# Kernel optimization log

Measured on AMD Instinct MI355X. Metric: run time of the kernel, lower is better.

Reference implementation:

```python
import jax, jax.numpy as jnp
import numpy as np

PAD = 0
CONST_NO = 10000   # ids > CONST_NO are variables
N_PRED = 50
B, S, G = 8, 64, 8
F, R, BMAX = 200000, 200, 3
K_F, K_R = 64, 32  # max fact / rule children per state


def _is_var(x):
    return x > CONST_NO


def setup_inputs() -> dict:
    key = jax.random.key(0)
    ks = jax.random.split(key, 12)
    # facts: (pred, arg0, arg1), preds in [1, N_PRED], args are constants
    fp = jax.random.randint(ks[0], (F, 1), 1, N_PRED + 1, dtype=jnp.int32)
    fa = jax.random.randint(ks[1], (F, 2), 1, CONST_NO + 1, dtype=jnp.int32)
    facts = jnp.concatenate([fp, fa], axis=1)
    fact_scores = jax.random.uniform(ks[2], (F,), jnp.float32, 0.1, 1.0)
    # rule heads: p(V1, V2) with V1 = CONST_NO+1, V2 = CONST_NO+2
    hp = jax.random.randint(ks[3], (R, 1), 1, N_PRED + 1, dtype=jnp.int32)
    heads = jnp.concatenate([hp,
                             jnp.full((R, 1), CONST_NO + 1, jnp.int32),
                             jnp.full((R, 1), CONST_NO + 2, jnp.int32)], axis=1)
    # rule bodies: args are head vars or fresh constants
    bp = jax.random.randint(ks[4], (R, BMAX, 1), 1, N_PRED + 1, dtype=jnp.int32)
    choice = jax.random.randint(ks[5], (R, BMAX, 2), 0, 3, dtype=jnp.int32)
    consts = jax.random.randint(ks[6], (R, BMAX, 2), 1, CONST_NO + 1, dtype=jnp.int32)
    bargs = jnp.where(choice == 0, CONST_NO + 1,
                      jnp.where(choice == 1, CONST_NO + 2, consts)).astype(jnp.int32)
    bodies = jnp.concatenate([bp, bargs], axis=2)
    rule_lens = jax.random.randint(ks[7], (R,), 1, BMAX + 1, dtype=jnp.int32)
    rule_scores = jax.random.uniform(ks[8], (R,), jnp.float32, 0.1, 1.0)
    # proof goals [B,S,G,3]: args mix of constants and query vars CONST_NO+3/+4
    gp = jax.random.randint(ks[9], (B, S, G, 1), 1, N_PRED + 1, dtype=jnp.int32)
    vch = jax.random.randint(ks[10], (B, S, G, 2), 0, 4, dtype=jnp.int32)
    gc = jax.random.randint(ks[11], (B, S, G, 2), 1, CONST_NO + 1, dtype=jnp.int32)
    gargs = jnp.where(vch == 0, CONST_NO + 3,
                      jnp.where(vch == 1, CONST_NO + 4, gc)).astype(jnp.int32)
    goals = jnp.concatenate([gp, gargs], axis=3)
    # variable number of live goals per state (tail padded)
    pos = jnp.arange(G)
    keep = jax.random.randint(jax.random.fold_in(key, 99), (B, S, 1), 1, G + 1, dtype=jnp.int32)
    goals = jnp.where(pos[None, None, :, None] < keep[..., None], goals, PAD)
    state_scores = jax.random.uniform(jax.random.fold_in(key, 7), (B, S), jnp.float32, 0.1, 1.0)
    return dict(proof_goals=goals, state_scores=state_scores, facts=facts,
                fact_scores=fact_scores, heads=heads, bodies=bodies,
                rule_lens=rule_lens, rule_scores=rule_scores)


def reference(proof_goals, state_scores, facts, fact_scores, heads, bodies, rule_lens, rule_scores):
    # ---- 1. SELECT: query = goal slot 0, remaining goals mask slot 0 ----
    q = proof_goals[:, :, 0]                         # [B,S,3]
    active = q[..., 0] != PAD                        # [B,S]
    remaining = proof_goals.at[:, :, 0, :].set(PAD)  # [B,S,G,3]
    qp, qa0, qa1 = q[..., 0], q[..., 1], q[..., 2]

    # ---- 2. RESOLVE FACTS: unify query against fact table ----
    m = ((qp[..., None] == facts[:, 0])
         & (_is_var(qa0)[..., None] | (qa0[..., None] == facts[:, 1]))
         & (_is_var(qa1)[..., None] | (qa1[..., None] == facts[:, 2]))
         & active[..., None])                        # [B,S,F]
    fvals, fidx = jax.lax.top_k(m.astype(jnp.int32), K_F)
    fact_success = fvals > 0                         # [B,S,K_f]
    mf = facts[fidx]                                 # [B,S,K_f,3]
    # substitute query variables with matched fact constants in remaining goals
    v0 = qa0[:, :, None, None, None]
    v1 = qa1[:, :, None, None, None]
    b0 = mf[..., 1][..., None, None]
    b1 = mf[..., 2][..., None, None]
    rem = remaining[:, :, None]                      # [B,S,1,G,3]
    fg = jnp.where(_is_var(v0) & (rem == v0), b0, rem)
    fg = jnp.where(_is_var(v1) & (fg == v1), b1, fg)  # [B,S,K_f,G,3]
    fsc = jnp.where(fact_success, state_scores[:, :, None] * fact_scores[fidx], 0.0)

    # ---- 3. RESOLVE RULES: unify query against rule heads, append bodies ----
    mr = ((qp[..., None] == heads[:, 0])
          & (_is_var(heads[:, 1]) | _is_var(qa0)[..., None] | (qa0[..., None] == heads[:, 1]))
          & (_is_var(heads[:, 2]) | _is_var(qa1)[..., None] | (qa1[..., None] == heads[:, 2]))
          & active[..., None])                       # [B,S,R]
    rvals, ridx = jax.lax.top_k(mr.astype(jnp.int32), K_R)
    rule_success = rvals > 0                         # [B,S,K_r]
    mh = heads[ridx]                                 # [B,S,K_r,3]
    body = bodies[ridx]                              # [B,S,K_r,BMAX,3]
    h0 = mh[..., 1][..., None, None]
    h1 = mh[..., 2][..., None, None]
    qa0b = qa0[:, :, None, None, None]
    qa1b = qa1[:, :, None, None, None]
    body = jnp.where(_is_var(h0) & (body == h0), qa0b, body)
    body = jnp.where(_is_var(h1) & (body == h1), qa1b, body)
    bmask = jnp.arange(BMAX) < rule_lens[ridx][..., None]    # [B,S,K_r,BMAX]
    body = jnp.where(bmask[..., None], body, PAD)
    rem_rest = jnp.broadcast_to(remaining[:, :, None, 1:1 + (G - BMAX)], (B, S, K_R, G - BMAX, 3))
    rg = jnp.concatenate([body, rem_rest], axis=3)   # [B,S,K_r,G,3]
    rsc = jnp.where(rule_success, state_scores[:, :, None] * rule_scores[ridx], 0.0)

    # ---- 4. PACK: flatten SxK children, compact successful ones to S states ----
    K = K_F + K_R
    all_goals = jnp.concatenate([fg, rg], axis=2).reshape(B, S * K, G, 3)
    all_succ = jnp.concatenate([fact_success, rule_success], axis=2).reshape(B, S * K)
    all_sc = jnp.concatenate([fsc, rsc], axis=2).reshape(B, S * K)
    pvals, pidx = jax.lax.top_k(all_succ.astype(jnp.int32), S)
    new_succ = pvals > 0                             # [B,S]
    new_goals = jnp.take_along_axis(all_goals, pidx[..., None, None], axis=1)
    # ---- 5. POSTPROCESS: zero out failed / padded states ----
    new_goals = jnp.where(new_succ[..., None, None], new_goals, PAD)
    new_scores = jnp.where(new_succ, jnp.take_along_axis(all_sc, pidx, axis=1), 0.0)
    return new_goals, new_scores
```

## Files before the change

kernel.cpp:

```cpp
#include <hip/hip_runtime.h>

#define PAD 0
#define CONST_NO 10000
#define Bn 8
#define Sn 64
#define Gn 8
#define Fn 200000
#define Rn 200
#define BMAXn 3
#define KF 64
#define KR 32

#define NBLK 196
#define CHB  1024

#define WS_STRIDE   128
#define OFF_RES     0
#define OFF_STARTS  (Bn * Sn * WS_STRIDE)
#define OFF_COUNTS  (OFF_STARTS + 64)
#define OFF_BHIST   (OFF_COUNTS + 64)
#define OFF_SORT    78336

__device__ __forceinline__ bool isv(int x) { return x > CONST_NO; }

__global__ __launch_bounds__(256) void hist_kernel(
    const int* __restrict__ facts, int* __restrict__ ws)
{
    __shared__ int h[64];
    const int t = threadIdx.x;
    if (t < 64) h[t] = 0;
    __syncthreads();
    const int f0 = blockIdx.x * CHB + t * 4;
    if (f0 + 3 < Fn) {
        const int4* p4 = (const int4*)(facts + 3 * f0);
        int4 a = p4[0], b4 = p4[1], c4 = p4[2];
        atomicAdd(&h[a.x],  1);
        atomicAdd(&h[a.w],  1);
        atomicAdd(&h[b4.z], 1);
        atomicAdd(&h[c4.y], 1);
    } else {
        #pragma unroll
        for (int u = 0; u < 4; ++u)
            if (f0 + u < Fn) atomicAdd(&h[facts[3 * (f0 + u)]], 1);
    }
    __syncthreads();
    if (t < 64) ws[OFF_BHIST + blockIdx.x * 64 + t] = h[t];
}

__global__ __launch_bounds__(256) void scatter_kernel(
    const int* __restrict__ facts, int* __restrict__ ws)
{
    __shared__ int predAll[CHB];
    __shared__ int coff[16][64];
    __shared__ int partAll[4][64];
    __shared__ int partPre[4][64];
    const int t = threadIdx.x;
    const int lane = t & 63, wv = t >> 6;
    const int B = blockIdx.x;

    for (int k = t; k < 16 * 64; k += 256) ((int*)coff)[k] = 0;

    {
        const int b0 = wv * 49, b1 = b0 + 49;
        int sA = 0, sP = 0;
        for (int b = b0; b < b1; ++b) {
            const int v = ws[OFF_BHIST + b * 64 + lane];
            sA += v;
            if (b < B) sP += v;
        }
        partAll[wv][lane] = sA;
        partPre[wv][lane] = sP;
    }

    const int f0 = B * CHB + t * 4;
    int pv[4], a0v[4], a1v[4];
    int nvalid = 0;
    if (f0 + 3 < Fn) {
        const int4* p4 = (const int4*)(facts + 3 * f0);
        int4 a = p4[0], b4 = p4[1], c4 = p4[2];
        pv[0] = a.x;  a0v[0] = a.y;  a1v[0] = a.z;
        pv[1] = a.w;  a0v[1] = b4.x; a1v[1] = b4.y;
        pv[2] = b4.z; a0v[2] = b4.w; a1v[2] = c4.x;
        pv[3] = c4.y; a0v[3] = c4.z; a1v[3] = c4.w;
        nvalid = 4;
    } else {
        #pragma unroll
        for (int u = 0; u < 4; ++u) {
            pv[u] = -1; a0v[u] = 0; a1v[u] = 0;
            if (f0 + u < Fn) {
                pv[u]  = facts[3 * (f0 + u)];
                a0v[u] = facts[3 * (f0 + u) + 1];
                a1v[u] = facts[3 * (f0 + u) + 2];
                nvalid = u + 1;
            }
        }
    }

    __syncthreads();

    const int c = t >> 4;
    #pragma unroll
    for (int u = 0; u < 4; ++u) {
        predAll[t * 4 + u] = pv[u];
        if (u < nvalid) atomicAdd(&coff[c][pv[u]], 1);
    }
    __syncthreads();

    if (t < 64) {
        const int tot = partAll[0][t] + partAll[1][t] + partAll[2][t] + partAll[3][t];
        const int pre = partPre[0][t] + partPre[1][t] + partPre[2][t] + partPre[3][t];
        int incl = tot;
        #pragma unroll
        for (int off = 1; off < 64; off <<= 1) {
            int n = __shfl_up(incl, off, 64);
            if (t >= off) incl += n;
        }
        const int start = incl - tot;
        if (B == 0) {
            ws[OFF_STARTS + t] = start;
            ws[OFF_COUNTS + t] = tot;
        }
        int run = start + pre;
        #pragma unroll
        for (int cc = 0; cc < 16; ++cc) {
            const int v = coff[cc][t];
            coff[cc][t] = run;
            run += v;
        }
    }
    __syncthreads();

    int4* sorted = (int4*)(ws + OFF_SORT);
    const int posb = (t & 15) * 4;
    #pragma unroll
    for (int u = 0; u < 4; ++u) {
        if (u < nvalid) {
            const int p = pv[u];
            int rank = 0;
            for (int j = 0; j < posb + u; ++j)
                rank += (predAll[c * 64 + j] == p);
            sorted[coff[c][p] + rank] = make_int4(a0v[u], a1v[u], f0 + u, 0);
        }
    }
}

__global__ __launch_bounds__(256) void match_kernel(
    const int* __restrict__ goals, const int* __restrict__ heads,
    int* __restrict__ ws)
{
    const int state = blockIdx.x;
    const int t = threadIdx.x;
    const int lane = t & 63, wv = t >> 6;
    __shared__ int wave_tot[4];

    const int* q = goals + state * (Gn * 3);
    const int qp = q[0], qa0 = q[1], qa1 = q[2];
    const bool active = (qp != PAD);
    const bool v0 = isv(qa0), v1 = isv(qa1);
    int* out = ws + OFF_RES + state * WS_STRIDE;

    const int st  = active ? ws[OFF_STARTS + qp] : 0;
    const int cnt = active ? ws[OFF_COUNTS + qp] : 0;
    const int4* S = (const int4*)(ws + OFF_SORT);

    if (v0 && v1) {
        const int n = (cnt < KF) ? cnt : KF;
        if (t < n) out[2 + t] = S[st + t].z;
        if (t == 0) out[0] = n;
    } else {
        int total = 0;
        for (int base = 0; base < cnt && total < KF; base += 1024) {
            const int k0 = base + t * 4;
            unsigned mbits = 0;
            int idxv[4];
            #pragma unroll
            for (int u = 0; u < 4; ++u) {
                idxv[u] = 0;
                if (k0 + u < cnt) {
                    const int4 f = S[st + k0 + u];
                    idxv[u] = f.z;
                    if ((v0 || f.x == qa0) && (v1 || f.y == qa1)) mbits |= (1u << u);
                }
            }
            const int c4 = __popc(mbits);

            int v = c4;
            #pragma unroll
            for (int off = 1; off < 64; off <<= 1) {
                int n = __shfl_up(v, off, 64);
                if (lane >= off) v += n;
            }
            if (lane == 63) wave_tot[wv] = v;
            __syncthreads();
            int excl = v - c4;
            #pragma unroll
            for (int w = 0; w < 4; ++w) if (w < wv) excl += wave_tot[w];
            const int ctot = wave_tot[0] + wave_tot[1] + wave_tot[2] + wave_tot[3];

            int pos = total + excl;
            #pragma unroll
            for (int u = 0; u < 4; ++u) {
                if (mbits & (1u << u)) {
                    if (pos < KF) out[2 + pos] = idxv[u];
                    pos++;
                }
            }
            total += ctot;
            __syncthreads();
        }
        if (t == 0) out[0] = (total < KF) ? total : KF;
    }

    int rcnt = 0;
    if (active && t < Rn) {
        const int h0 = heads[3 * t], h1 = heads[3 * t + 1], h2 = heads[3 * t + 2];
        if ((h0 == qp) && (isv(h1) || v0 || qa0 == h1)
                       && (isv(h2) || v1 || qa1 == h2))
            rcnt = 1;
    }
    __syncthreads();
    int v = rcnt;
    #pragma unroll
    for (int off = 1; off < 64; off <<= 1) {
        int n = __shfl_up(v, off, 64);
        if (lane >= off) v += n;
    }
    if (lane == 63) wave_tot[wv] = v;
    __syncthreads();
    int excl = v - rcnt;
    #pragma unroll
    for (int w = 0; w < 4; ++w) if (w < wv) excl += wave_tot[w];
    const int rtot = wave_tot[0] + wave_tot[1] + wave_tot[2] + wave_tot[3];
    if (rcnt && excl < KR) out[66 + excl] = t;
    if (t == 0) out[1] = (rtot < KR) ? rtot : KR;
}

__global__ __launch_bounds__(256) void select_kernel(
    const int* __restrict__ goals, const float* __restrict__ ss,
    const int* __restrict__ facts, const float* __restrict__ fsc,
    const int* __restrict__ heads, const int* __restrict__ bodies,
    const int* __restrict__ rlens, const float* __restrict__ rsc,
    const int* __restrict__ ws, float* __restrict__ outp)
{
    const int b = blockIdx.x >> 3;
    const int k = blockIdx.x & 7;
    const int t = threadIdx.x;
    __shared__ int pref[Sn + 1];
    __shared__ int nf_s[Sn];

    if (t < Sn) {
        const int* w = ws + OFF_RES + (b * Sn + t) * WS_STRIDE;
        const int nf = w[0];
        nf_s[t] = nf;
        int val = nf + w[1];
        int incl = val;
        #pragma unroll
        for (int off = 1; off < 64; off <<= 1) {
            int n = __shfl_up(incl, off, 64);
            if (t >= off) incl += n;
        }
        pref[t + 1] = incl;
        if (t == 0) pref[0] = 0;
    }
    __syncthreads();
    const int total = pref[Sn];

    if (t < 64) {
        const int i = k * 8 + (t >> 3), g = t & 7;
        int trip[3] = {PAD, PAD, PAD};
        if (i < total) {
            int lo = 0, hi = Sn - 1;
            while (lo < hi) {
                const int mid = (lo + hi) >> 1;
                if (pref[mid + 1] <= i) lo = mid + 1; else hi = mid;
            }
            const int s = lo, j = i - pref[s];
            const int* w = ws + OFF_RES + (b * Sn + s) * WS_STRIDE;
            const int* q = goals + (b * Sn + s) * (Gn * 3);
            const int qa0 = q[1], qa1 = q[2];
            if (j < nf_s[s]) {
                const int fi = w[2 + j];
                const int f1 = facts[3 * fi + 1], f2 = facts[3 * fi + 2];
                if (g >= 1) {
                    #pragma unroll
                    for (int c = 0; c < 3; ++c) {
                        int x = q[g * 3 + c];
                        if (isv(qa0) && x == qa0) x = f1;
                        else if (isv(qa1) && x == qa1) x = f2;
                        trip[c] = x;
                    }
                }
            } else {
                const int ri = w[66 + (j - nf_s[s])];
                const int h1 = heads[3 * ri + 1], h2 = heads[3 * ri + 2];
                const int len = rlens[ri];
                if (g < BMAXn) {
                    if (g < len) {
                        #pragma unroll
                        for (int c = 0; c < 3; ++c) {
                            int x = bodies[(ri * BMAXn + g) * 3 + c];
                            if (isv(h1) && x == h1) x = qa0;
                            if (isv(h2) && x == h2) x = qa1;
                            trip[c] = x;
                        }
                    }
                } else {
                    trip[0] = q[(g - 2) * 3 + 0];
                    trip[1] = q[(g - 2) * 3 + 1];
                    trip[2] = q[(g - 2) * 3 + 2];
                }
            }
        }
        float* o = outp + ((b * Sn + i) * Gn + g) * 3;
        o[0] = (float)trip[0];
        o[1] = (float)trip[1];
        o[2] = (float)trip[2];
    } else if (t >= 128 && t < 136) {
        const int i = k * 8 + (t - 128);
        float sc = 0.f;
        if (i < total) {
            int lo = 0, hi = Sn - 1;
            while (lo < hi) {
                const int mid = (lo + hi) >> 1;
                if (pref[mid + 1] <= i) lo = mid + 1; else hi = mid;
            }
            const int s = lo, j = i - pref[s];
            const int* w = ws + OFF_RES + (b * Sn + s) * WS_STRIDE;
            const float stt = ss[b * Sn + s];
            if (j < nf_s[s]) sc = stt * fsc[w[2 + j]];
            else             sc = stt * rsc[w[66 + (j - nf_s[s])]];
        }
        outp[Bn * Sn * Gn * 3 + b * Sn + i] = sc;
    }
}

extern "C" void kernel_launch(void* const* d_in, const int* in_sizes, int n_in,
                              void* d_out, int out_size, void* d_ws, size_t ws_size,
                              hipStream_t stream) {
    const int*   goals  = (const int*)  d_in[0];
    const float* ss     = (const float*)d_in[1];
    const int*   facts  = (const int*)  d_in[2];
    const float* fsc    = (const float*)d_in[3];
    const int*   heads  = (const int*)  d_in[4];
    const int*   bodies = (const int*)  d_in[5];
    const int*   rlens  = (const int*)  d_in[6];
    const float* rsc    = (const float*)d_in[7];
    int*   ws   = (int*)d_ws;
    float* outp = (float*)d_out;

    hist_kernel   <<<NBLK,    256, 0, stream>>>(facts, ws);
    scatter_kernel<<<NBLK,    256, 0, stream>>>(facts, ws);
    match_kernel  <<<Bn * Sn, 256, 0, stream>>>(goals, heads, ws);
    select_kernel <<<Bn * 8,  256, 0, stream>>>(goals, ss, facts, fsc, heads,
                                                bodies, rlens, rsc, ws, outp);
}
```

Measured before the change: 95.33 us.

## Use ballot-based ranking, larger chunks, and packed int2 sorted fact entries

The histogram and scatter kernels now use wave ballots to compute per-predicate counts and in-wave ranks. This replaces shared-memory atomics and the serial O(n) rank loop. Chunk size doubles so half as many blocks run. Sorted entries shrink from int4 to int2 by packing both 14-bit arguments into one word, and matching uses a masked XOR compare. This halves the bandwidth of the sorted array. The packing assumes constants fit in 14 bits; variable ids up to about 10004 still fit.

```diff
diff --git a/kernel.cpp b/kernel.cpp
--- a/kernel.cpp
+++ b/kernel.cpp
@@ -11,57 +11,78 @@
 #define KF 64
 #define KR 32
 
-#define NBLK 196
-#define CHB  1024
+#define NBLK 98
+#define CHB  2048
 
 #define WS_STRIDE   128
 #define OFF_RES     0
 #define OFF_STARTS  (Bn * Sn * WS_STRIDE)
 #define OFF_COUNTS  (OFF_STARTS + 64)
 #define OFF_BHIST   (OFF_COUNTS + 64)
-#define OFF_SORT    78336
+#define OFF_SORT    71936
 
 __device__ __forceinline__ bool isv(int x) { return x > CONST_NO; }
+
+__device__ __forceinline__ unsigned long long same_pred_mask(int p, unsigned long long valid)
+{
+    unsigned long long mask = valid;
+    #pragma unroll
+    for (int bit = 0; bit < 6; ++bit) {
+        const unsigned long long b = __ballot((p >> bit) & 1);
+        mask &= ((p >> bit) & 1) ? b : ~b;
+    }
+    return mask;
+}
 
 __global__ __launch_bounds__(256) void hist_kernel(
     const int* __restrict__ facts, int* __restrict__ ws)
 {
-    __shared__ int h[64];
-    const int t = threadIdx.x;
-    if (t < 64) h[t] = 0;
-    __syncthreads();
-    const int f0 = blockIdx.x * CHB + t * 4;
-    if (f0 + 3 < Fn) {
-        const int4* p4 = (const int4*)(facts + 3 * f0);
-        int4 a = p4[0], b4 = p4[1], c4 = p4[2];
-        atomicAdd(&h[a.x],  1);
-        atomicAdd(&h[a.w],  1);
-        atomicAdd(&h[b4.z], 1);
-        atomicAdd(&h[c4.y], 1);
-    } else {
+    __shared__ int cnt[32][64];
+    const int t = threadIdx.x, lane = t & 63, wv = t >> 6;
+    const int B = blockIdx.x;
+
+    for (int k = t; k < 32 * 64; k += 256) ((int*)cnt)[k] = 0;
+
+    int pv[8];
+    #pragma unroll
+    for (int k = 0; k < 8; ++k) {
+        const int c = wv * 8 + k;
+        const int i = B * CHB + c * 64 + lane;
+        pv[k] = (i < Fn) ? facts[3 * i] : -1;
+    }
+    __syncthreads();
+
+    const unsigned long long lmlt = (1ull << lane) - 1ull;
+    #pragma unroll
+    for (int k = 0; k < 8; ++k) {
+        const int c = wv * 8 + k;
+        const unsigned long long valid = __ballot(pv[k] >= 0);
+        const unsigned long long mask = same_pred_mask(pv[k], valid);
+        if (pv[k] >= 0 && (mask & lmlt) == 0)
+            cnt[c][pv[k]] = (int)__popcll(mask);
+    }
+    __syncthreads();
+    if (t < 64) {
+        int s = 0;
         #pragma unroll
-        for (int u = 0; u < 4; ++u)
-            if (f0 + u < Fn) atomicAdd(&h[facts[3 * (f0 + u)]], 1);
-    }
-    __syncthreads();
-    if (t < 64) ws[OFF_BHIST + blockIdx.x * 64 + t] = h[t];
+        for (int c = 0; c < 32; ++c) s += cnt[c][t];
+        ws[OFF_BHIST + B * 64 + t] = s;
+    }
 }
 
 __global__ __launch_bounds__(256) void scatter_kernel(
     const int* __restrict__ facts, int* __restrict__ ws)
 {
-    __shared__ int predAll[CHB];
-    __shared__ int coff[16][64];
+    __shared__ int cnt[32][64];
     __shared__ int partAll[4][64];
     __shared__ int partPre[4][64];
-    const int t = threadIdx.x;
-    const int lane = t & 63, wv = t >> 6;
+    const int t = threadIdx.x, lane = t & 63, wv = t >> 6;
     const int B = blockIdx.x;
 
-    for (int k = t; k < 16 * 64; k += 256) ((int*)coff)[k] = 0;
+    for (int k = t; k < 32 * 64; k += 256) ((int*)cnt)[k] = 0;
 
     {
-        const int b0 = wv * 49, b1 = b0 + 49;
+        const int b0 = wv * 25, b1 = (b0 + 25 < NBLK) ? b0 + 25 : NBLK;
         int sA = 0, sP = 0;
         for (int b = b0; b < b1; ++b) {
             const int v = ws[OFF_BHIST + b * 64 + lane];
@@ -72,37 +93,32 @@
         partPre[wv][lane] = sP;
     }
 
-    const int f0 = B * CHB + t * 4;
-    int pv[4], a0v[4], a1v[4];
-    int nvalid = 0;
-    if (f0 + 3 < Fn) {
-        const int4* p4 = (const int4*)(facts + 3 * f0);
-        int4 a = p4[0], b4 = p4[1], c4 = p4[2];
-        pv[0] = a.x;  a0v[0] = a.y;  a1v[0] = a.z;
-        pv[1] = a.w;  a0v[1] = b4.x; a1v[1] = b4.y;
-        pv[2] = b4.z; a0v[2] = b4.w; a1v[2] = c4.x;
-        pv[3] = c4.y; a0v[3] = c4.z; a1v[3] = c4.w;
-        nvalid = 4;
-    } else {
-        #pragma unroll
-        for (int u = 0; u < 4; ++u) {
-            pv[u] = -1; a0v[u] = 0; a1v[u] = 0;
-            if (f0 + u < Fn) {
-                pv[u]  = facts[3 * (f0 + u)];
-                a0v[u] = facts[3 * (f0 + u) + 1];
-                a1v[u] = facts[3 * (f0 + u) + 2];
-                nvalid = u + 1;
-            }
-        }
-    }
-
-    __syncthreads();
-
-    const int c = t >> 4;
-    #pragma unroll
-    for (int u = 0; u < 4; ++u) {
-        predAll[t * 4 + u] = pv[u];
-        if (u < nvalid) atomicAdd(&coff[c][pv[u]], 1);
+    int pv[8], pk[8];
+    #pragma unroll
+    for (int k = 0; k < 8; ++k) {
+        const int c = wv * 8 + k;
+        const int i = B * CHB + c * 64 + lane;
+        int p = -1, a0 = 0, a1 = 0;
+        if (i < Fn) {
+            p  = facts[3 * i];
+            a0 = facts[3 * i + 1];
+            a1 = facts[3 * i + 2];
+        }
+        pv[k] = p;
+        pk[k] = (a0 << 14) | a1;
+    }
+    __syncthreads();
+
+    const unsigned long long lmlt = (1ull << lane) - 1ull;
+    int rk[8];
+    #pragma unroll
+    for (int k = 0; k < 8; ++k) {
+        const int c = wv * 8 + k;
+        const unsigned long long valid = __ballot(pv[k] >= 0);
+        const unsigned long long mask = same_pred_mask(pv[k], valid);
+        rk[k] = (int)__popcll(mask & lmlt);
+        if (pv[k] >= 0 && (mask & lmlt) == 0)
+            cnt[c][pv[k]] = (int)__popcll(mask);
     }
     __syncthreads();
 
@@ -122,24 +138,21 @@
         }
         int run = start + pre;
         #pragma unroll
-        for (int cc = 0; cc < 16; ++cc) {
-            const int v = coff[cc][t];
-            coff[cc][t] = run;
+        for (int c = 0; c < 32; ++c) {
+            const int v = cnt[c][t];
+            cnt[c][t] = run;
             run += v;
         }
     }
     __syncthreads();
 
-    int4* sorted = (int4*)(ws + OFF_SORT);
-    const int posb = (t & 15) * 4;
-    #pragma unroll
-    for (int u = 0; u < 4; ++u) {
-        if (u < nvalid) {
-            const int p = pv[u];
-            int rank = 0;
-            for (int j = 0; j < posb + u; ++j)
-                rank += (predAll[c * 64 + j] == p);
-            sorted[coff[c][p] + rank] = make_int4(a0v[u], a1v[u], f0 + u, 0);
+    int2* sorted = (int2*)(ws + OFF_SORT);
+    #pragma unroll
+    for (int k = 0; k < 8; ++k) {
+        if (pv[k] >= 0) {
+            const int c = wv * 8 + k;
+            const int i = B * CHB + c * 64 + lane;
+            sorted[cnt[c][pv[k]] + rk[k]] = make_int2(pk[k], i);
         }
     }
 }
@@ -161,13 +174,15 @@
 
     const int st  = active ? ws[OFF_STARTS + qp] : 0;
     const int cnt = active ? ws[OFF_COUNTS + qp] : 0;
-    const int4* S = (const int4*)(ws + OFF_SORT);
+    const int2* S = (const int2*)(ws + OFF_SORT);
 
     if (v0 && v1) {
         const int n = (cnt < KF) ? cnt : KF;
-        if (t < n) out[2 + t] = S[st + t].z;
+        if (t < n) out[2 + t] = S[st + t].y;
         if (t == 0) out[0] = n;
     } else {
+        const int qv = (v0 ? 0 : (qa0 << 14)) | (v1 ? 0 : qa1);
+        const int qm = (v0 ? 0 : (0x3FFF << 14)) | (v1 ? 0 : 0x3FFF);
         int total = 0;
         for (int base = 0; base < cnt && total < KF; base += 1024) {
             const int k0 = base + t * 4;
@@ -177,9 +192,9 @@
             for (int u = 0; u < 4; ++u) {
                 idxv[u] = 0;
                 if (k0 + u < cnt) {
-                    const int4 f = S[st + k0 + u];
-                    idxv[u] = f.z;
-                    if ((v0 || f.x == qa0) && (v1 || f.y == qa1)) mbits |= (1u << u);
+                    const int2 f = S[st + k0 + u];
+                    idxv[u] = f.y;
+                    if (((f.x ^ qv) & qm) == 0) mbits |= (1u << u);
                 }
             }
             const int c4 = __popc(mbits);
```

Result: no change. 93.72 us (-1.7%).
